# Kernel optimization log

Measured on AMD Instinct MI355X. Metric: run time of the kernel, lower is better.

Reference implementation:

```python
import jax, jax.numpy as jnp
import numpy as np

B, P, C_IN, C = 2, 100000, 23, 64
H, W = 512, 512
S = H * W  # num voxels per batch element
EPS_BN1, EPS_BN2 = 1e-5, 1e-3


def setup_inputs() -> dict:
    key = jax.random.key(0)
    ks = jax.random.split(key, 16)
    valid = jax.random.uniform(ks[0], (B, P)) > 0.1
    inp = {
        "points_xyz": jax.random.normal(ks[1], (B, P, 3), jnp.float32),
        "points_feature": jax.random.normal(ks[2], (B, P, C_IN), jnp.float32),
        "points_mask": valid.astype(jnp.float32),
        "indices": jax.random.randint(ks[3], (B, P), 0, S, jnp.int32),
        "paddings": (1 - valid.astype(jnp.int32)),
        "voxel_xyz": jax.random.uniform(ks[4], (B, P, 3), jnp.float32) * 511.0,
        # PointNet linear (bias=False) + BatchNorm1d params (eval-style stats)
        "w_pn": jax.random.normal(ks[5], (C_IN, C), jnp.float32) * 0.1,
        "bn1_gamma": jax.random.uniform(ks[6], (C,), jnp.float32, 0.5, 1.5),
        "bn1_beta": jax.random.normal(ks[7], (C,), jnp.float32) * 0.1,
        "bn1_mean": jax.random.normal(ks[8], (C,), jnp.float32) * 0.1,
        "bn1_var": jax.random.uniform(ks[9], (C,), jnp.float32, 0.5, 1.5),
        # res1: Conv2d 1x1 (bias=False) + BatchNorm2d
        "conv_w": jax.random.normal(ks[10], (C, C), jnp.float32) * 0.05,  # [out,in]
        "bn2_gamma": jax.random.uniform(ks[11], (C,), jnp.float32, 0.5, 1.5),
        "bn2_beta": jax.random.normal(ks[12], (C,), jnp.float32) * 0.1,
        "bn2_mean": jax.random.normal(ks[13], (C,), jnp.float32) * 0.1,
        "bn2_var": jax.random.uniform(ks[14], (C,), jnp.float32, 0.5, 1.5),
    }
    return inp


def reference(points_xyz, points_feature, points_mask, indices, paddings, voxel_xyz,
              w_pn, bn1_gamma, bn1_beta, bn1_mean, bn1_var,
              conv_w, bn2_gamma, bn2_beta, bn2_mean, bn2_var):
    # ---- PointNet: Linear -> BN -> ReLU -> mask ----
    x = jnp.einsum("bpi,io->bpo", points_feature, w_pn)
    x = (x - bn1_mean) * jax.lax.rsqrt(bn1_var + EPS_BN1) * bn1_gamma + bn1_beta
    x = jax.nn.relu(x) * points_mask[..., None]  # [B,P,C]

    # ---- batched unsorted segment max (padded points -> dummy segment) ----
    valid = paddings == 0
    batch_off = jnp.arange(B, dtype=jnp.int32)[:, None] * S
    flat_ids = jnp.where(valid, indices + batch_off, B * S).reshape(-1)
    voxels = jax.ops.segment_max(x.reshape(B * P, C), flat_ids,
                                 num_segments=B * S + 1)[: B * S]
    voxels = jnp.where(jnp.isneginf(voxels), 0.0, voxels)  # empty voxels -> 0
    v = voxels.reshape(B, H, W, C)

    # ---- res1: 1x1 conv + BN + ReLU (NHWC layout) ----
    v = jnp.einsum("bhwc,oc->bhwo", v, conv_w)
    v = (v - bn2_mean) * jax.lax.rsqrt(bn2_var + EPS_BN2) * bn2_gamma + bn2_beta
    v = jax.nn.relu(v)

    # torch: voxels[B,C,H,W].permute(0,3,2,1) -> [B,W,H,C]; x indexes W, y indexes H
    im = jnp.transpose(v, (0, 2, 1, 3))  # [B,W,H,C]

    # ---- bilinear gather at voxel_xyz[..., :2] ----
    xq = voxel_xyz[..., 0]
    yq = voxel_xyz[..., 1]
    x0 = jnp.clip(jnp.floor(xq).astype(jnp.int32), 0, W - 1)
    x1 = jnp.clip(x0 + 1, 0, W - 1)
    y0 = jnp.clip(jnp.floor(yq).astype(jnp.int32), 0, H - 1)
    y1 = jnp.clip(y0 + 1, 0, H - 1)
    bidx = jnp.arange(B, dtype=jnp.int32)[:, None]
    Ia = im[bidx, x0, y0]
    Ib = im[bidx, x0, y1]
    Ic = im[bidx, x1, y0]
    Id = im[bidx, x1, y1]
    x0f, x1f = x0.astype(xq.dtype), x1.astype(xq.dtype)
    y0f, y1f = y0.astype(yq.dtype), y1.astype(yq.dtype)
    wa = (x1f - xq) * (y1f - yq)
    wb = (x1f - xq) * (yq - y0f)
    wc = (xq - x0f) * (y1f - yq)
    wd = (xq - x0f) * (yq - y0f)
    points_out = (wa[..., None] * Ia + wb[..., None] * Ib
                  + wc[..., None] * Ic + wd[..., None] * Id)  # [B,P,C]
    return points_out
```

## Files before the change

### kernel.cpp

```cpp
#include <hip/hip_runtime.h>
#include <hip/hip_bf16.h>

#define B_ 2
#define P_ 100000
#define CIN_ 23
#define C_ 64
#define H_ 512
#define W_ 512
#define S_ (H_*W_)
#define NPT_ (B_*P_)
#define NVOX_ (B_*S_)

typedef __attribute__((ext_vector_type(8))) short short8;
typedef __attribute__((ext_vector_type(4))) float f32x4;
typedef __attribute__((ext_vector_type(4))) int i32x4;
typedef __attribute__((ext_vector_type(4), aligned(4))) float f32x4u;

__device__ inline unsigned short f2bf(float f) {
    union { __hip_bfloat16 h; unsigned short u; } cv;
    cv.h = __float2bfloat16(f);
    return cv.u;
}
__device__ inline float bf2f(unsigned short u) {
    union { unsigned int i; float f; } cv;
    cv.i = ((unsigned int)u) << 16;
    return cv.f;
}
__device__ inline void bf2x(unsigned int u, float& lo, float& hi) {
    union { unsigned int i; float f; } a, b;
    a.i = u << 16;
    b.i = u & 0xffff0000u;
    lo = a.f; hi = b.f;
}

__global__ __launch_bounds__(256) void k_clear(int* __restrict__ cnt)
{
    int i = (blockIdx.x * 256 + threadIdx.x) * 4;
    if (i > NVOX_) return;
    *(i32x4*)(cnt + i) = (i32x4){0, 0, 0, 0};
}

__global__ __launch_bounds__(256) void k_hist(
    const int* __restrict__ indices,
    const int* __restrict__ paddings,
    int* __restrict__ cnt,
    int* __restrict__ rank)
{
    int t4 = (blockIdx.x * 256 + threadIdx.x) * 4;
    if (t4 >= NPT_) return;
    i32x4 idx4 = *(const i32x4*)(indices + t4);
    i32x4 pad4 = *(const i32x4*)(paddings + t4);
    int vb = (t4 / P_) * S_;
    #pragma unroll
    for (int j = 0; j < 4; ++j)
        if (pad4[j] == 0)
            rank[t4 + j] = atomicAdd(&cnt[vb + idx4[j]], 1);
}

__global__ __launch_bounds__(256) void k_offsets(
    const int* __restrict__ cnt,
    int* __restrict__ cur,
    int* __restrict__ rid,
    int* __restrict__ off_c,
    int* __restrict__ cnt_c,
    int* __restrict__ gcursor,
    const float* __restrict__ conv_w,
    const float* __restrict__ w_pn,
    const float* __restrict__ g1, const float* __restrict__ b1,
    const float* __restrict__ m1, const float* __restrict__ v1,
    const float* __restrict__ g2, const float* __restrict__ b2,
    const float* __restrict__ m2, const float* __restrict__ v2,
    unsigned short* __restrict__ cwb,
    unsigned short* __restrict__ wpb,
    float* __restrict__ o1v,
    float* __restrict__ scv, float* __restrict__ shv)
{
    if (blockIdx.x >= 512) {
        int t = threadIdx.x;
        if (t < 64) {
            float s = g1[t] * rsqrtf(v1[t] + 1e-5f);
            o1v[t] = b1[t] - m1[t] * s;
            float s2 = g2[t] * rsqrtf(v2[t] + 1e-3f);
            scv[t] = s2;
            shv[t] = b2[t] - m2[t] * s2;
        }
        #pragma unroll
        for (int e = 0; e < 16; ++e) {
            int idx  = t * 16 + e;
            int f    = idx >> 9;
            int lane = (idx >> 3) & 63;
            int j    = idx & 7;
            int tq = f >> 1, ks = f & 1;
            int row = lane & 15, grp = lane >> 4;
            cwb[idx] = f2bf(conv_w[(tq * 16 + row) * 64 + ks * 32 + grp * 8 + j]);
        }
        #pragma unroll
        for (int e = 0; e < 8; ++e) {
            int idx  = t * 8 + e;
            int tq   = idx >> 9;
            int lane = (idx >> 3) & 63;
            int j    = idx & 7;
            int row = lane & 15, grp = lane >> 4;
            int n = tq * 16 + row;
            int k = grp * 8 + j;
            float s1n = g1[n] * rsqrtf(v1[n] + 1e-5f);
            wpb[idx] = (k < CIN_) ? f2bf(w_pn[k * C_ + n] * s1n) : 0;
        }
        return;
    }

    __shared__ int lds_c[256], lds_o[256];
    __shared__ int sbase_c, sbase_o;
    int tid  = threadIdx.x;
    int base = blockIdx.x * 1024 + tid * 4;
    i32x4 c = *(const i32x4*)(cnt + base);
    int o0 = c[0] > 0, o1 = c[1] > 0, o2 = c[2] > 0, o3 = c[3] > 0;
    int sc1 = c[0] + c[1], sc2 = sc1 + c[2], sc3 = sc2 + c[3];
    int so1 = o0 + o1,     so2 = so1 + o2,   so3 = so2 + o3;
    lds_c[tid] = sc3;
    lds_o[tid] = so3;
    __syncthreads();
    #pragma unroll
    for (int d = 1; d < 256; d <<= 1) {
        int vc = (tid >= d) ? lds_c[tid - d] : 0;
        int vo = (tid >= d) ? lds_o[tid - d] : 0;
        __syncthreads();
        if (tid >= d) { lds_c[tid] += vc; lds_o[tid] += vo; }
        __syncthreads();
    }
    if (tid == 0) {
        sbase_c = atomicAdd(&gcursor[0], lds_c[255]);
        sbase_o = atomicAdd(&gcursor[1], lds_o[255]);
    }
    __syncthreads();
    int oc = sbase_c + (tid == 0 ? 0 : lds_c[tid - 1]);
    int oo = sbase_o + (tid == 0 ? 0 : lds_o[tid - 1]);
    i32x4 e, ridv;
    e[0] = oc; e[1] = oc + c[0]; e[2] = oc + sc1; e[3] = oc + sc2;
    ridv[0] = o0 ? oo            : -1;
    ridv[1] = o1 ? oo + so1 - o1 : -1;
    ridv[2] = o2 ? oo + so2 - o2 : -1;
    ridv[3] = o3 ? oo + so3 - o3 : -1;
    *(i32x4*)(cur + base) = e;
    *(i32x4*)(rid + base) = ridv;
    #pragma unroll
    for (int i = 0; i < 4; ++i) {
        if (ridv[i] >= 0) {
            off_c[ridv[i]] = e[i];
            cnt_c[ridv[i]] = c[i];
        }
    }
}

__global__ __launch_bounds__(256) void k_ptid(
    const int* __restrict__ indices,
    const int* __restrict__ paddings,
    const int* __restrict__ cur,
    const int* __restrict__ rank,
    int* __restrict__ ptid)
{
    int pt = blockIdx.x * 256 + threadIdx.x;
    if (pt >= NPT_) return;
    if (paddings[pt] != 0) return;
    int v = (pt / P_) * S_ + indices[pt];
    ptid[cur[v] + rank[pt]] = pt;
}

__global__ __launch_bounds__(256) void k_redconv(
    const float* __restrict__ feat,
    const int* __restrict__ ptid,
    const int* __restrict__ off_c,
    const int* __restrict__ cnt_c,
    const int* __restrict__ gcursor,
    const unsigned short* __restrict__ wpb,
    const float* __restrict__ o1v,
    const unsigned short* __restrict__ cwb,
    const float* __restrict__ scv, const float* __restrict__ shv,
    unsigned short* __restrict__ grid_c)
{
    __shared__ unsigned short lds[4][16][64];

    int lane = threadIdx.x & 63;
    int wv   = threadIdx.x >> 6;
    int wid  = (blockIdx.x * 256 + threadIdx.x) >> 6;
    int r0   = wid * 16;
    int nocc = gcursor[1];
    if (r0 >= nocc) return;

    int col = lane & 15;
    int grp = lane >> 4;

    int rA    = r0 + col;
    bool livA = rA < nocc;
    int ciA   = livA ? cnt_c[rA] : 0;
    int oiA   = livA ? off_c[rA] : 0;

    int ci4[4];
    #pragma unroll
    for (int r = 0; r < 4; ++r) ci4[r] = __shfl(ciA, grp * 4 + r);

    short8 bz[4];
    #pragma unroll
    for (int t = 0; t < 4; ++t)
        bz[t] = *(const short8*)(wpb + ((size_t)t * 64 + lane) * 8);

    f32x4 mx[4];
    #pragma unroll
    for (int t = 0; t < 4; ++t) mx[t] = (f32x4){-1e30f, -1e30f, -1e30f, -1e30f};

    for (int j = 0; ; ++j) {
        if (!__any(j < ciA)) break;
        int jj = j < ciA ? j : 0;
        int pt = ptid[oiA + jj];
        const float* f = feat + (size_t)pt * CIN_;
        short8 a = (short8){0,0,0,0,0,0,0,0};
        if (grp < 3) {
            f32x4u v0 = *(const f32x4u*)(f + grp * 8);
            f32x4u v1 = *(const f32x4u*)(f + grp * 8 + 4);
            #pragma unroll
            for (int jx = 0; jx < 4; ++jx) {
                int k0 = grp * 8 + jx;
                int k1 = k0 + 4;
                a[jx]     = (short)(k0 < CIN_ ? f2bf(v0[jx]) : 0);
                a[jx + 4] = (short)(k1 < CIN_ ? f2bf(v1[jx]) : 0);
            }
        }
        #pragma unroll
        for (int t = 0; t < 4; ++t) {
            f32x4 zt = __builtin_amdgcn_mfma_f32_16x16x32_bf16(
                a, bz[t], (f32x4){0.f, 0.f, 0.f, 0.f}, 0, 0, 0);
            #pragma unroll
            for (int r = 0; r < 4; ++r)
                if (j < ci4[r]) mx[t][r] = fmaxf(mx[t][r], zt[r]);
        }
    }

    #pragma unroll
    for (int t = 0; t < 4; ++t) {
        float o1 = o1v[t * 16 + col];
        #pragma unroll
        for (int r = 0; r < 4; ++r) {
            int row = grp * 4 + r;
            float val = fmaxf(mx[t][r] + o1, 0.f);
            lds[wv][row][(t * 16 + col) ^ ((row & 7) << 3)] = f2bf(val);
        }
    }

    short8 a2[2];
    #pragma unroll
    for (int ks = 0; ks < 2; ++ks)
        a2[ks] = *(const short8*)&lds[wv][col][(ks * 32 + grp * 8) ^ ((col & 7) << 3)];

    short8 bfrag[4][2];
    #pragma unroll
    for (int t = 0; t < 4; ++t)
        #pragma unroll
        for (int ks = 0; ks < 2; ++ks)
            bfrag[t][ks] = *(const short8*)(cwb + ((size_t)(t * 2 + ks) * 64 + lane) * 8);

    f32x4 acc[4];
    #pragma unroll
    for (int t = 0; t < 4; ++t) acc[t] = (f32x4){0.f, 0.f, 0.f, 0.f};
    #pragma unroll
    for (int t = 0; t < 4; ++t) {
        acc[t] = __builtin_amdgcn_mfma_f32_16x16x32_bf16(a2[0], bfrag[t][0], acc[t], 0, 0, 0);
        acc[t] = __builtin_amdgcn_mfma_f32_16x16x32_bf16(a2[1], bfrag[t][1], acc[t], 0, 0, 0);
    }

    float sc[4], sh[4];
    #pragma unroll
    for (int t = 0; t < 4; ++t) {
        int n = t * 16 + col;
        sc[t] = scv[n];
        sh[t] = shv[n];
    }
    #pragma unroll
    for (int rq = 0; rq < 4; ++rq) {
        int rr = r0 + grp * 4 + rq;
        if (rr < nocc) {
            unsigned short* op = grid_c + (size_t)rr * C_;
            #pragma unroll
            for (int t = 0; t < 4; ++t) {
                float val = fmaxf(acc[t][rq] * sc[t] + sh[t], 0.f);
                op[t * 16 + col] = f2bf(val);
            }
        }
    }
}

__global__ __launch_bounds__(256) void k_gather32(
    const unsigned short* __restrict__ grid_c,
    const int* __restrict__ rid,
    const float* __restrict__ vxyz,
    const float* __restrict__ shv,
    float* __restrict__ out)
{
    int lane = threadIdx.x & 63;
    int q    = lane >> 4;
    int ch   = (lane & 15) * 4;
    int gw   = (blockIdx.x * 256 + threadIdx.x) >> 6;
    int p0   = gw * 32;
    if (p0 >= NPT_) return;

    f32x4 cstv = *(const f32x4*)(shv + ch);
    #pragma unroll
    for (int j = 0; j < 4; ++j) cstv[j] = fmaxf(cstv[j], 0.f);

    const unsigned short* gc = grid_c + ch;

    #pragma unroll
    for (int it = 0; it < 8; ++it) {
        int pt = p0 + it * 4 + q;
        int b  = pt / P_;
        float xq = vxyz[(size_t)pt * 3 + 0];
        float yq = vxyz[(size_t)pt * 3 + 1];
        int x0 = (int)floorf(xq); x0 = min(max(x0, 0), W_ - 1);
        int x1 = min(x0 + 1, W_ - 1);
        int y0 = (int)floorf(yq); y0 = min(max(y0, 0), H_ - 1);
        int y1 = min(y0 + 1, H_ - 1);
        float x0f = (float)x0, x1f = (float)x1, y0f = (float)y0, y1f = (float)y1;
        float wa = (x1f - xq) * (y1f - yq);
        float wb = (x1f - xq) * (yq - y0f);
        float wc = (xq - x0f) * (y1f - yq);
        float wd = (xq - x0f) * (yq - y0f);

        int ia = y0 * W_ + x0, ib = y1 * W_ + x0, ic = y0 * W_ + x1, id = y1 * W_ + x1;
        const int* rb = rid + (size_t)b * S_;

        int ra = rb[ia], rbn = rb[ib], rc = rb[ic], rd = rb[id];
        uint2 Ra = *(const uint2*)(gc + (size_t)max(ra,  0) * C_);
        uint2 Rb = *(const uint2*)(gc + (size_t)max(rbn, 0) * C_);
        uint2 Rc = *(const uint2*)(gc + (size_t)max(rc,  0) * C_);
        uint2 Rd = *(const uint2*)(gc + (size_t)max(rd,  0) * C_);

        float A0,A1,A2,A3, B0,B1,B2,B3, C0,C1,C2,C3, D0,D1,D2,D3;
        bf2x(Ra.x, A0, A1); bf2x(Ra.y, A2, A3);
        bf2x(Rb.x, B0, B1); bf2x(Rb.y, B2, B3);
        bf2x(Rc.x, C0, C1); bf2x(Rc.y, C2, C3);
        bf2x(Rd.x, D0, D1); bf2x(Rd.y, D2, D3);

        bool oa = ra >= 0, ob = rbn >= 0, oc = rc >= 0, od = rd >= 0;
        f32x4 res;
        res[0] = wa * (oa ? A0 : cstv[0]) + wb * (ob ? B0 : cstv[0])
               + wc * (oc ? C0 : cstv[0]) + wd * (od ? D0 : cstv[0]);
        res[1] = wa * (oa ? A1 : cstv[1]) + wb * (ob ? B1 : cstv[1])
               + wc * (oc ? C1 : cstv[1]) + wd * (od ? D1 : cstv[1]);
        res[2] = wa * (oa ? A2 : cstv[2]) + wb * (ob ? B2 : cstv[2])
               + wc * (oc ? C2 : cstv[2]) + wd * (od ? D2 : cstv[2]);
        res[3] = wa * (oa ? A3 : cstv[3]) + wb * (ob ? B3 : cstv[3])
               + wc * (oc ? C3 : cstv[3]) + wd * (od ? D3 : cstv[3]);

        *(f32x4*)(out + (size_t)pt * C_ + ch) = res;
    }
}

extern "C" void kernel_launch(void* const* d_in, const int* in_sizes, int n_in,
                              void* d_out, int out_size, void* d_ws, size_t ws_size,
                              hipStream_t stream)
{
    const float* feat     = (const float*)d_in[1];
    const int*   indices  = (const int*)d_in[3];
    const int*   paddings = (const int*)d_in[4];
    const float* vxyz     = (const float*)d_in[5];
    const float* w_pn     = (const float*)d_in[6];
    const float* g1       = (const float*)d_in[7];
    const float* b1       = (const float*)d_in[8];
    const float* m1       = (const float*)d_in[9];
    const float* v1       = (const float*)d_in[10];
    const float* cw       = (const float*)d_in[11];
    const float* g2       = (const float*)d_in[12];
    const float* b2       = (const float*)d_in[13];
    const float* m2       = (const float*)d_in[14];
    const float* v2       = (const float*)d_in[15];

    char* p = (char*)d_ws;
    unsigned short* grid_c = (unsigned short*)p;  p += (size_t)NPT_ * C_ * 2;
    int* cnt   = (int*)p;  p += (size_t)NVOX_ * 4;
    int* gcur  = (int*)p;  p += 16;
    int* cur   = (int*)p;  p += (size_t)NVOX_ * 4;
    int* rid   = (int*)p;  p += (size_t)NVOX_ * 4;
    int* off_c = (int*)p;  p += (size_t)NPT_ * 4;
    int* cnt_c = (int*)p;  p += (size_t)NPT_ * 4;
    int* ptid  = (int*)p;  p += (size_t)NPT_ * 4;
    int* rank  = (int*)p;  p += (size_t)NPT_ * 4;
    unsigned short* cwb = (unsigned short*)p;  p += 8 * 64 * 8 * 2;
    unsigned short* wpb = (unsigned short*)p;  p += 4 * 64 * 8 * 2;
    float* o1v = (float*)p;  p += 64 * 4;
    float* scv = (float*)p;  p += 64 * 4;
    float* shv = (float*)p;

    k_clear<<<513, 256, 0, stream>>>(cnt);

    k_hist<<<196, 256, 0, stream>>>(indices, paddings, cnt, rank);

    k_offsets<<<513, 256, 0, stream>>>(cnt, cur, rid, off_c, cnt_c, gcur,
        cw, w_pn, g1, b1, m1, v1, g2, b2, m2, v2,
        cwb, wpb, o1v, scv, shv);

    k_ptid<<<(NPT_ + 255) / 256, 256, 0, stream>>>(indices, paddings, cur, rank, ptid);

    k_redconv<<<3125, 256, 0, stream>>>(feat, ptid, off_c, cnt_c, gcur,
        wpb, o1v, cwb, scv, shv, grid_c);

    k_gather32<<<1563, 256, 0, stream>>>(grid_c, rid, vxyz, shv, (float*)d_out);
}
```

Before: 76.58 us.

## Fuse clear, histogram, offsets and ptid kernels into one cooperative kernel

Merges the four front-end kernels (clear counts, histogram with atomics, scan/offsets plus parameter folding, point-id scatter) into a single cooperative kernel of 513 blocks separated by grid-wide syncs. This removes three kernel launches and their inter-kernel gaps. It also replaces integer divisions by P with a comparison. The cost is three grid barriers, and the histogram and ptid phases run on fewer threads per point. Correctness relies on all 513 blocks being co-resident.

New measurement: 231.3 us. +202.0%, slower.

```diff
diff --git a/kernel.cpp b/kernel.cpp
--- a/kernel.cpp
+++ b/kernel.cpp
@@ -1,5 +1,8 @@
 #include <hip/hip_runtime.h>
 #include <hip/hip_bf16.h>
+#include <hip/hip_cooperative_groups.h>
+
+namespace cg = cooperative_groups;
 
 #define B_ 2
 #define P_ 100000
@@ -33,37 +36,17 @@
     lo = a.f; hi = b.f;
 }
 
-__global__ __launch_bounds__(256) void k_clear(int* __restrict__ cnt)
-{
-    int i = (blockIdx.x * 256 + threadIdx.x) * 4;
-    if (i > NVOX_) return;
-    *(i32x4*)(cnt + i) = (i32x4){0, 0, 0, 0};
-}
-
-__global__ __launch_bounds__(256) void k_hist(
+__global__ __launch_bounds__(256) void k_front(
     const int* __restrict__ indices,
     const int* __restrict__ paddings,
     int* __restrict__ cnt,
-    int* __restrict__ rank)
-{
-    int t4 = (blockIdx.x * 256 + threadIdx.x) * 4;
-    if (t4 >= NPT_) return;
-    i32x4 idx4 = *(const i32x4*)(indices + t4);
-    i32x4 pad4 = *(const i32x4*)(paddings + t4);
-    int vb = (t4 / P_) * S_;
-    #pragma unroll
-    for (int j = 0; j < 4; ++j)
-        if (pad4[j] == 0)
-            rank[t4 + j] = atomicAdd(&cnt[vb + idx4[j]], 1);
-}
-
-__global__ __launch_bounds__(256) void k_offsets(
-    const int* __restrict__ cnt,
+    int* __restrict__ rank,
     int* __restrict__ cur,
     int* __restrict__ rid,
     int* __restrict__ off_c,
     int* __restrict__ cnt_c,
     int* __restrict__ gcursor,
+    int* __restrict__ ptid,
     const float* __restrict__ conv_w,
     const float* __restrict__ w_pn,
     const float* __restrict__ g1, const float* __restrict__ b1,
@@ -75,8 +58,34 @@
     float* __restrict__ o1v,
     float* __restrict__ scv, float* __restrict__ shv)
 {
-    if (blockIdx.x >= 512) {
-        int t = threadIdx.x;
+    cg::grid_group grid = cg::this_grid();
+    int tid = threadIdx.x;
+    int bid = blockIdx.x;
+    int gt  = bid * 256 + tid;
+
+    {
+        int i = gt * 4;
+        if (i <= NVOX_)
+            *(i32x4*)(cnt + i) = (i32x4){0, 0, 0, 0};
+    }
+    grid.sync();
+
+    {
+        int t4 = gt * 4;
+        if (t4 < NPT_) {
+            i32x4 idx4 = *(const i32x4*)(indices + t4);
+            i32x4 pad4 = *(const i32x4*)(paddings + t4);
+            int vb = (t4 >= P_) ? S_ : 0;
+            #pragma unroll
+            for (int j = 0; j < 4; ++j)
+                if (pad4[j] == 0)
+                    rank[t4 + j] = atomicAdd(&cnt[vb + idx4[j]], 1);
+        }
+    }
+    grid.sync();
+
+    if (bid >= 512) {
+        int t = tid;
         if (t < 64) {
             float s = g1[t] * rsqrtf(v1[t] + 1e-5f);
             o1v[t] = b1[t] - m1[t] * s;
@@ -106,64 +115,61 @@
             float s1n = g1[n] * rsqrtf(v1[n] + 1e-5f);
             wpb[idx] = (k < CIN_) ? f2bf(w_pn[k * C_ + n] * s1n) : 0;
         }
-        return;
-    }
-
-    __shared__ int lds_c[256], lds_o[256];
-    __shared__ int sbase_c, sbase_o;
-    int tid  = threadIdx.x;
-    int base = blockIdx.x * 1024 + tid * 4;
-    i32x4 c = *(const i32x4*)(cnt + base);
-    int o0 = c[0] > 0, o1 = c[1] > 0, o2 = c[2] > 0, o3 = c[3] > 0;
-    int sc1 = c[0] + c[1], sc2 = sc1 + c[2], sc3 = sc2 + c[3];
-    int so1 = o0 + o1,     so2 = so1 + o2,   so3 = so2 + o3;
-    lds_c[tid] = sc3;
-    lds_o[tid] = so3;
-    __syncthreads();
-    #pragma unroll
-    for (int d = 1; d < 256; d <<= 1) {
-        int vc = (tid >= d) ? lds_c[tid - d] : 0;
-        int vo = (tid >= d) ? lds_o[tid - d] : 0;
+    } else {
+        __shared__ int lds_c[256], lds_o[256];
+        __shared__ int sbase_c, sbase_o;
+        int base = bid * 1024 + tid * 4;
+        i32x4 c = *(const i32x4*)(cnt + base);
+        int o0 = c[0] > 0, o1 = c[1] > 0, o2 = c[2] > 0, o3 = c[3] > 0;
+        int sc1 = c[0] + c[1], sc2 = sc1 + c[2], sc3 = sc2 + c[3];
+        int so1 = o0 + o1,     so2 = so1 + o2,   so3 = so2 + o3;
+        lds_c[tid] = sc3;
+        lds_o[tid] = so3;
         __syncthreads();
-        if (tid >= d) { lds_c[tid] += vc; lds_o[tid] += vo; }
+        #pragma unroll
+        for (int d = 1; d < 256; d <<= 1) {
+            int vc = (tid >= d) ? lds_c[tid - d] : 0;
+            int vo = (tid >= d) ? lds_o[tid - d] : 0;
+            __syncthreads();
+            if (tid >= d) { lds_c[tid] += vc; lds_o[tid] += vo; }
+            __syncthreads();
+        }
+        if (tid == 0) {
+            sbase_c = atomicAdd(&gcursor[0], lds_c[255]);
+            sbase_o = atomicAdd(&gcursor[1], lds_o[255]);
+        }
         __syncthreads();
-    }
-    if (tid == 0) {
-        sbase_c = atomicAdd(&gcursor[0], lds_c[255]);
-        sbase_o = atomicAdd(&gcursor[1], lds_o[255]);
-    }
-    __syncthreads();
-    int oc = sbase_c + (tid == 0 ? 0 : lds_c[tid - 1]);
-    int oo = sbase_o + (tid == 0 ? 0 : lds_o[tid - 1]);
-    i32x4 e, ridv;
-    e[0] = oc; e[1] = oc + c[0]; e[2] = oc + sc1; e[3] = oc + sc2;
-    ridv[0] = o0 ? oo            : -1;
-    ridv[1] = o1 ? oo + so1 - o1 : -1;
-    ridv[2] = o2 ? oo + so2 - o2 : -1;
-    ridv[3] = o3 ? oo + so3 - o3 : -1;
-    *(i32x4*)(cur + base) = e;
-    *(i32x4*)(rid + base) = ridv;
-    #pragma unroll
-    for (int i = 0; i < 4; ++i) {
-        if (ridv[i] >= 0) {
-            off_c[ridv[i]] = e[i];
-            cnt_c[ridv[i]] = c[i];
-        }
-    }
-}
-
-__global__ __launch_bounds__(256) void k_ptid(
-    const int* __restrict__ indices,
-    const int* __restrict__ paddings,
-    const int* __restrict__ cur,
-    const int* __restrict__ rank,
-    int* __restrict__ ptid)
-{
-    int pt = blockIdx.x * 256 + threadIdx.x;
-    if (pt >= NPT_) return;
-    if (paddings[pt] != 0) return;
-    int v = (pt / P_) * S_ + indices[pt];
-    ptid[cur[v] + rank[pt]] = pt;
+        int oc = sbase_c + (tid == 0 ? 0 : lds_c[tid - 1]);
+        int oo = sbase_o + (tid == 0 ? 0 : lds_o[tid - 1]);
+        i32x4 e, ridv;
+        e[0] = oc; e[1] = oc + c[0]; e[2] = oc + sc1; e[3] = oc + sc2;
+        ridv[0] = o0 ? oo            : -1;
+        ridv[1] = o1 ? oo + so1 - o1 : -1;
+        ridv[2] = o2 ? oo + so2 - o2 : -1;
+        ridv[3] = o3 ? oo + so3 - o3 : -1;
+        *(i32x4*)(cur + base) = e;
+        *(i32x4*)(rid + base) = ridv;
+        #pragma unroll
+        for (int i = 0; i < 4; ++i) {
+            if (ridv[i] >= 0) {
+                off_c[ridv[i]] = e[i];
+                cnt_c[ridv[i]] = c[i];
+            }
+        }
+    }
+    grid.sync();
+
+    {
+        int p0 = gt * 2;
+        #pragma unroll
+        for (int j = 0; j < 2; ++j) {
+            int pt = p0 + j;
+            if (pt < NPT_ && paddings[pt] == 0) {
+                int v = ((pt >= P_) ? S_ : 0) + indices[pt];
+                ptid[cur[v] + rank[pt]] = pt;
+            }
+        }
+    }
 }
 
 __global__ __launch_bounds__(256) void k_redconv(
@@ -311,7 +317,7 @@
     #pragma unroll
     for (int it = 0; it < 8; ++it) {
         int pt = p0 + it * 4 + q;
-        int b  = pt / P_;
+        int b  = (pt >= P_);
         float xq = vxyz[(size_t)pt * 3 + 0];
         float yq = vxyz[(size_t)pt * 3 + 1];
         int x0 = (int)floorf(xq); x0 = min(max(x0, 0), W_ - 1);
@@ -389,15 +395,15 @@
     float* scv = (float*)p;  p += 64 * 4;
     float* shv = (float*)p;
 
-    k_clear<<<513, 256, 0, stream>>>(cnt);
-
-    k_hist<<<196, 256, 0, stream>>>(indices, paddings, cnt, rank);
-
-    k_offsets<<<513, 256, 0, stream>>>(cnt, cur, rid, off_c, cnt_c, gcur,
-        cw, w_pn, g1, b1, m1, v1, g2, b2, m2, v2,
-        cwb, wpb, o1v, scv, shv);
-
-    k_ptid<<<(NPT_ + 255) / 256, 256, 0, stream>>>(indices, paddings, cur, rank, ptid);
+    void* args[] = {
+        (void*)&indices, (void*)&paddings, (void*)&cnt, (void*)&rank,
+        (void*)&cur, (void*)&rid, (void*)&off_c, (void*)&cnt_c, (void*)&gcur,
+        (void*)&ptid,
+        (void*)&cw, (void*)&w_pn, (void*)&g1, (void*)&b1, (void*)&m1, (void*)&v1,
+        (void*)&g2, (void*)&b2, (void*)&m2, (void*)&v2,
+        (void*)&cwb, (void*)&wpb, (void*)&o1v, (void*)&scv, (void*)&shv
+    };
+    hipLaunchCooperativeKernel((void*)k_front, dim3(513), dim3(256), args, 0, stream);
 
     k_redconv<<<3125, 256, 0, stream>>>(feat, ptid, off_c, cnt_c, gcur,
         wpb, o1v, cwb, scv, shv, grid_c);
```
